# Kernel tuning notes

Hardware: AMD Instinct MI355X
Metric: run time of the kernel (lower is better)

The kernel has to match this reference:

```python
import jax, jax.numpy as jnp
import numpy as np

N_LEVELS = 16
F_PER_LEVEL = 2
LOG2_HASH = 19
HASH_SIZE = 1 << LOG2_HASH
HASH_MASK = HASH_SIZE - 1
BASE_RES = 16
FINEST_RES = 512
N_POINTS = 1_000_000

_growth = np.exp((np.log(FINEST_RES) - np.log(BASE_RES)) / (N_LEVELS - 1))
RESOLUTIONS = [int(BASE_RES * _growth ** l) for l in range(N_LEVELS)]
# corner offsets in the torch loop order: dz outer, dy middle, dx inner
OFFSETS = np.array([[dx, dy, dz] for dz in (0, 1) for dy in (0, 1) for dx in (0, 1)], dtype=np.uint32)  # [8,3]
PRIMES = np.array([1, 2654435761, 805459861], dtype=np.uint32)


def setup_inputs() -> dict:
    key = jax.random.key(0)
    k1, k2 = jax.random.split(key)
    x = jax.random.normal(k1, (N_POINTS, 3), dtype=jnp.float32)
    # matches nn.init.uniform_(tbl.weight, -1e-4, 1e-4)
    tables = jax.random.uniform(k2, (N_LEVELS, HASH_SIZE, F_PER_LEVEL), minval=-1e-4, maxval=1e-4, dtype=jnp.float32)
    return {"x": x, "tables": tables}


def _encode_level(x_scaled, resolution, table):
    # x_scaled: [N,3] in [0,1]; table: [HASH_SIZE, F]
    xg = x_scaled * resolution
    xfloor = jnp.floor(xg)
    frac = xg - xfloor                                   # [N,3]
    offs = jnp.asarray(OFFSETS)                          # [8,3] uint32
    corners = xfloor.astype(jnp.uint32)[:, None, :] + offs[None]  # [N,8,3]
    primes = jnp.asarray(PRIMES)
    # spatial hash: XOR of coord*prime, mod 2^19 (power of two -> low-bit mask; uint32 wraparound is exact here)
    h = (corners[..., 0] * primes[0]) ^ (corners[..., 1] * primes[1]) ^ (corners[..., 2] * primes[2])
    idx = (h & jnp.uint32(HASH_MASK)).astype(jnp.int32)  # [N,8]
    feats = table[idx]                                   # [N,8,F]
    off_f = offs.astype(x_scaled.dtype)                  # [8,3]
    # trilinear weights: prod over dims of (frac if offset==1 else 1-frac)
    w = jnp.prod(off_f[None] * frac[:, None, :] + (1.0 - off_f[None]) * (1.0 - frac[:, None, :]), axis=-1)  # [N,8]
    return jnp.sum(w[..., None] * feats, axis=1)         # [N,F]


def reference(x, tables):
    x_min = x.min(axis=0, keepdims=True)
    x_max = x.max(axis=0, keepdims=True)
    x_scaled = (x - x_min) / (x_max - x_min + 1e-8)
    outs = [_encode_level(x_scaled, float(RESOLUTIONS[l]), tables[l]) for l in range(N_LEVELS)]
    return jnp.concatenate(outs, axis=-1)                # [N, 32]
```

## Files before the change

### kernel.cpp

```cpp
#include <hip/hip_runtime.h>
#include <cmath>

constexpr unsigned HASH_SIZE = 1u << 19;
constexpr unsigned HASH_MASK = HASH_SIZE - 1u;
constexpr unsigned P2 = 2654435761u;
constexpr unsigned P3 = 805459861u;
constexpr int NKEYS = 65536;
constexpr int NSHARD = 8;

struct ResArr { float r[16]; };
typedef float f4 __attribute__((ext_vector_type(4)));

__global__ __launch_bounds__(256) void he_minmax1(const float* __restrict__ x, int n,
                                                  float* __restrict__ part) {
    int tid = blockIdx.x * blockDim.x + threadIdx.x;
    int stride = gridDim.x * blockDim.x;
    float mn0 = INFINITY, mn1 = INFINITY, mn2 = INFINITY;
    float mx0 = -INFINITY, mx1 = -INFINITY, mx2 = -INFINITY;
    for (int i = tid; i < n; i += stride) {
        float a = x[3 * i + 0];
        float b = x[3 * i + 1];
        float c = x[3 * i + 2];
        mn0 = fminf(mn0, a); mx0 = fmaxf(mx0, a);
        mn1 = fminf(mn1, b); mx1 = fmaxf(mx1, b);
        mn2 = fminf(mn2, c); mx2 = fmaxf(mx2, c);
    }
    #pragma unroll
    for (int off = 32; off > 0; off >>= 1) {
        mn0 = fminf(mn0, __shfl_down(mn0, off));
        mn1 = fminf(mn1, __shfl_down(mn1, off));
        mn2 = fminf(mn2, __shfl_down(mn2, off));
        mx0 = fmaxf(mx0, __shfl_down(mx0, off));
        mx1 = fmaxf(mx1, __shfl_down(mx1, off));
        mx2 = fmaxf(mx2, __shfl_down(mx2, off));
    }
    __shared__ float s[6][4];
    int w = threadIdx.x >> 6;
    if ((threadIdx.x & 63) == 0) {
        s[0][w] = mn0; s[1][w] = mn1; s[2][w] = mn2;
        s[3][w] = mx0; s[4][w] = mx1; s[5][w] = mx2;
    }
    __syncthreads();
    if (threadIdx.x == 0) {
        float* p = part + 6 * blockIdx.x;
        p[0] = fminf(fminf(s[0][0], s[0][1]), fminf(s[0][2], s[0][3]));
        p[1] = fminf(fminf(s[1][0], s[1][1]), fminf(s[1][2], s[1][3]));
        p[2] = fminf(fminf(s[2][0], s[2][1]), fminf(s[2][2], s[2][3]));
        p[3] = fmaxf(fmaxf(s[3][0], s[3][1]), fmaxf(s[3][2], s[3][3]));
        p[4] = fmaxf(fmaxf(s[4][0], s[4][1]), fmaxf(s[4][2], s[4][3]));
        p[5] = fmaxf(fmaxf(s[5][0], s[5][1]), fmaxf(s[5][2], s[5][3]));
    }
}

__global__ __launch_bounds__(256) void he_minmax2(const float* __restrict__ part,
                                                  float* __restrict__ mm) {
    int t = threadIdx.x;
    const float* p = part + 6 * t;
    float mn0 = p[0], mn1 = p[1], mn2 = p[2];
    float mx0 = p[3], mx1 = p[4], mx2 = p[5];
    #pragma unroll
    for (int off = 32; off > 0; off >>= 1) {
        mn0 = fminf(mn0, __shfl_down(mn0, off));
        mn1 = fminf(mn1, __shfl_down(mn1, off));
        mn2 = fminf(mn2, __shfl_down(mn2, off));
        mx0 = fmaxf(mx0, __shfl_down(mx0, off));
        mx1 = fmaxf(mx1, __shfl_down(mx1, off));
        mx2 = fmaxf(mx2, __shfl_down(mx2, off));
    }
    __shared__ float s[6][4];
    int w = t >> 6;
    if ((t & 63) == 0) {
        s[0][w] = mn0; s[1][w] = mn1; s[2][w] = mn2;
        s[3][w] = mx0; s[4][w] = mx1; s[5][w] = mx2;
    }
    __syncthreads();
    if (t == 0) {
        mm[0] = fminf(fminf(s[0][0], s[0][1]), fminf(s[0][2], s[0][3]));
        mm[1] = fminf(fminf(s[1][0], s[1][1]), fminf(s[1][2], s[1][3]));
        mm[2] = fminf(fminf(s[2][0], s[2][1]), fminf(s[2][2], s[2][3]));
        mm[3] = fmaxf(fmaxf(s[3][0], s[3][1]), fmaxf(s[3][2], s[3][3]));
        mm[4] = fmaxf(fmaxf(s[4][0], s[4][1]), fmaxf(s[4][2], s[4][3]));
        mm[5] = fmaxf(fmaxf(s[5][0], s[5][1]), fmaxf(s[5][2], s[5][3]));
    }
}

__device__ __forceinline__ unsigned spread5(unsigned v) {
    return (v & 1u) | ((v & 2u) << 2) | ((v & 4u) << 4) | ((v & 8u) << 6) | ((v & 16u) << 8);
}

__global__ __launch_bounds__(256) void he_keys(const float* __restrict__ x, int n,
                                               const float* __restrict__ mm,
                                               unsigned* __restrict__ planes,
                                               unsigned short* __restrict__ keyA) {
    int i = blockIdx.x * 256 + threadIdx.x;
    if (i >= n) return;
    float den0 = (mm[3] - mm[0]) + 1e-8f;
    float den1 = (mm[4] - mm[1]) + 1e-8f;
    float den2 = (mm[5] - mm[2]) + 1e-8f;
    float xs = (x[3 * i + 0] - mm[0]) / den0;
    float ys = (x[3 * i + 1] - mm[1]) / den1;
    float zs = (x[3 * i + 2] - mm[2]) / den2;
    unsigned kx = min(63u, (unsigned)(xs * 64.0f));
    unsigned ky = min(31u, (unsigned)(ys * 32.0f));
    unsigned kz = min(31u, (unsigned)(zs * 32.0f));
    unsigned key = ((kx >> 5) << 15)
                 | (spread5(kx & 31u) << 2)
                 | (spread5(ky) << 1)
                 | spread5(kz);
    keyA[i] = (unsigned short)key;
    atomicAdd(&planes[(i & (NSHARD - 1)) * NKEYS + key], 1u);
}

__global__ __launch_bounds__(256) void he_scanShards(unsigned* __restrict__ planes,
                                                     unsigned* __restrict__ keytot) {
    int k = blockIdx.x * 256 + threadIdx.x;
    unsigned c[NSHARD];
    #pragma unroll
    for (int s = 0; s < NSHARD; ++s) c[s] = planes[s * NKEYS + k];
    unsigned run = 0;
    #pragma unroll
    for (int s = 0; s < NSHARD; ++s) {
        planes[s * NKEYS + k] = run;
        run += c[s];
    }
    keytot[k] = run;
}

__global__ __launch_bounds__(256) void he_scanA(unsigned* __restrict__ keytot,
                                                unsigned* __restrict__ bsum) {
    __shared__ unsigned s[256];
    int tid = threadIdx.x;
    int g = blockIdx.x * 256 + tid;
    unsigned v = keytot[g];
    s[tid] = v;
    __syncthreads();
    #pragma unroll
    for (int off = 1; off < 256; off <<= 1) {
        unsigned t = (tid >= off) ? s[tid - off] : 0u;
        __syncthreads();
        s[tid] += t;
        __syncthreads();
    }
    keytot[g] = s[tid] - v;
    if (tid == 255) bsum[blockIdx.x] = s[255];
}

__global__ __launch_bounds__(256) void he_scanB(unsigned* __restrict__ bsum) {
    __shared__ unsigned s[256];
    int tid = threadIdx.x;
    unsigned v = bsum[tid];
    s[tid] = v;
    __syncthreads();
    #pragma unroll
    for (int off = 1; off < 256; off <<= 1) {
        unsigned t = (tid >= off) ? s[tid - off] : 0u;
        __syncthreads();
        s[tid] += t;
        __syncthreads();
    }
    bsum[tid] = s[tid] - v;
}

__global__ __launch_bounds__(256) void he_scanC(unsigned* __restrict__ planes,
                                                const unsigned* __restrict__ keytot,
                                                const unsigned* __restrict__ bsum) {
    int g = blockIdx.x * 256 + threadIdx.x;
    unsigned base = keytot[g] + bsum[blockIdx.x];
    #pragma unroll
    for (int s = 0; s < NSHARD; ++s) planes[s * NKEYS + g] += base;
}

__global__ __launch_bounds__(256) void he_scatter(const unsigned short* __restrict__ keyA,
                                                  const float* __restrict__ x, int n,
                                                  const float* __restrict__ mm,
                                                  unsigned* __restrict__ planes,
                                                  f4* __restrict__ xsorted) {
    int i = blockIdx.x * 256 + threadIdx.x;
    if (i >= n) return;
    float den0 = (mm[3] - mm[0]) + 1e-8f;
    float den1 = (mm[4] - mm[1]) + 1e-8f;
    float den2 = (mm[5] - mm[2]) + 1e-8f;
    float xs = (x[3 * i + 0] - mm[0]) / den0;
    float ys = (x[3 * i + 1] - mm[1]) / den1;
    float zs = (x[3 * i + 2] - mm[2]) / den2;
    unsigned k = keyA[i];
    unsigned pos = atomicAdd(&planes[(i & (NSHARD - 1)) * NKEYS + k], 1u);
    f4 v;
    v.x = xs; v.y = ys; v.z = zs; v.w = __uint_as_float((unsigned)i);
    xsorted[pos] = v;
}

__device__ __forceinline__ void enc_core(float xs, float ys, float zs,
                                         const float* __restrict__ tables,
                                         const ResArr& res, float o[32]) {
    #pragma unroll
    for (int l = 0; l < 16; ++l) {
        float R = res.r[l];
        float xg = xs * R, yg = ys * R, zg = zs * R;
        float fx = floorf(xg), fy = floorf(yg), fz = floorf(zg);
        float tx = xg - fx, ty = yg - fy, tz = zg - fz;
        unsigned cx = (unsigned)fx, cy = (unsigned)fy, cz = (unsigned)fz;

        unsigned hx0 = cx,      hx1 = cx + 1u;
        unsigned hy0 = cy * P2, hy1 = hy0 + P2;
        unsigned hz0 = cz * P3, hz1 = hz0 + P3;

        const float2* __restrict__ T = (const float2*)tables + (size_t)l * HASH_SIZE;

        float2 f000 = T[(hx0 ^ hy0 ^ hz0) & HASH_MASK];
        float2 f100 = T[(hx1 ^ hy0 ^ hz0) & HASH_MASK];
        float2 f010 = T[(hx0 ^ hy1 ^ hz0) & HASH_MASK];
        float2 f110 = T[(hx1 ^ hy1 ^ hz0) & HASH_MASK];
        float2 f001 = T[(hx0 ^ hy0 ^ hz1) & HASH_MASK];
        float2 f101 = T[(hx1 ^ hy0 ^ hz1) & HASH_MASK];
        float2 f011 = T[(hx0 ^ hy1 ^ hz1) & HASH_MASK];
        float2 f111 = T[(hx1 ^ hy1 ^ hz1) & HASH_MASK];

        float wx0 = 1.0f - tx, wx1 = tx;
        float wy0 = 1.0f - ty, wy1 = ty;
        float wz0 = 1.0f - tz, wz1 = tz;

        float w000 = wx0 * wy0 * wz0;
        float w100 = wx1 * wy0 * wz0;
        float w010 = wx0 * wy1 * wz0;
        float w110 = wx1 * wy1 * wz0;
        float w001 = wx0 * wy0 * wz1;
        float w101 = wx1 * wy0 * wz1;
        float w011 = wx0 * wy1 * wz1;
        float w111 = wx1 * wy1 * wz1;

        float a0 = w000 * f000.x;
        float a1 = w000 * f000.y;
        a0 += w100 * f100.x;  a1 += w100 * f100.y;
        a0 += w010 * f010.x;  a1 += w010 * f010.y;
        a0 += w110 * f110.x;  a1 += w110 * f110.y;
        a0 += w001 * f001.x;  a1 += w001 * f001.y;
        a0 += w101 * f101.x;  a1 += w101 * f101.y;
        a0 += w011 * f011.x;  a1 += w011 * f011.y;
        a0 += w111 * f111.x;  a1 += w111 * f111.y;

        o[2 * l + 0] = a0;
        o[2 * l + 1] = a1;
    }
}

__device__ __forceinline__ int swz_block(int b, int nwg) {
    int q = nwg >> 3, r = nwg & 7;
    int xcd = b & 7, kk = b >> 3;
    return (xcd < r ? xcd * (q + 1) : r * (q + 1) + (xcd - r) * q) + kk;
}

__global__ __launch_bounds__(256) void he_encode_scatter(const f4* __restrict__ xsorted,
                                                         const float* __restrict__ tables,
                                                         float* __restrict__ out, int n, ResArr res) {
    int sb = swz_block(blockIdx.x, gridDim.x);
    int j = sb * 256 + threadIdx.x;
    if (j >= n) return;
    f4 p = xsorted[j];
    int i = (int)__float_as_uint(p.w);
    float o[32];
    enc_core(p.x, p.y, p.z, tables, res, o);
    float* op = out + (size_t)i * 32;
    #pragma unroll
    for (int k = 0; k < 8; ++k) {
        f4 v;
        v.x = o[4 * k + 0]; v.y = o[4 * k + 1]; v.z = o[4 * k + 2]; v.w = o[4 * k + 3];
        *(f4*)(op + 4 * k) = v;
    }
}

__global__ __launch_bounds__(256) void he_encode_plain(const float* __restrict__ x,
                                                       const float* __restrict__ tables,
                                                       const float* __restrict__ mm,
                                                       float* __restrict__ out, int n, ResArr res) {
    int i = blockIdx.x * 256 + threadIdx.x;
    if (i >= n) return;
    float den0 = (mm[3] - mm[0]) + 1e-8f;
    float den1 = (mm[4] - mm[1]) + 1e-8f;
    float den2 = (mm[5] - mm[2]) + 1e-8f;
    float xs = (x[3 * i + 0] - mm[0]) / den0;
    float ys = (x[3 * i + 1] - mm[1]) / den1;
    float zs = (x[3 * i + 2] - mm[2]) / den2;
    float o[32];
    enc_core(xs, ys, zs, tables, res, o);
    float* op = out + (size_t)i * 32;
    #pragma unroll
    for (int k = 0; k < 8; ++k) {
        f4 v;
        v.x = o[4 * k + 0]; v.y = o[4 * k + 1]; v.z = o[4 * k + 2]; v.w = o[4 * k + 3];
        __builtin_nontemporal_store(v, (f4*)(op + 4 * k));
    }
}

extern "C" void kernel_launch(void* const* d_in, const int* in_sizes, int n_in,
                              void* d_out, int out_size, void* d_ws, size_t ws_size,
                              hipStream_t stream) {
    const float* x = (const float*)d_in[0];
    const float* tables = (const float*)d_in[1];
    float* out = (float*)d_out;
    int n = in_sizes[0] / 3;

    char* w = (char*)d_ws;
    float*          mm      = (float*)w;
    float*          part    = (float*)(w + 4096);
    unsigned*       bsum    = (unsigned*)(w + 16384);
    unsigned*       keytot  = (unsigned*)(w + 32768);
    unsigned*       planes  = (unsigned*)(w + 524288);
    unsigned short* keyA    = (unsigned short*)(w + 0x300000);
    f4*             xsorted = (f4*)(w + 0x500000);

    const size_t NEED1 = 0x500000 + (size_t)16777216;
    int tier = (ws_size >= NEED1) ? 1 : 0;
    if (n > (1 << 20)) tier = 0;

    ResArr res;
    double growth = exp((log(512.0) - log(16.0)) / 15.0);
    for (int l = 0; l < 16; ++l) {
        res.r[l] = (float)(int)(16.0 * pow(growth, (double)l));
    }

    int blocks = (n + 255) / 256;

    he_minmax1<<<256, 256, 0, stream>>>(x, n, part);
    he_minmax2<<<1, 256, 0, stream>>>(part, mm);

    if (tier >= 1) {
        hipMemsetAsync(planes, 0, (size_t)NSHARD * NKEYS * 4, stream);
        he_keys<<<blocks, 256, 0, stream>>>(x, n, mm, planes, keyA);
        he_scanShards<<<NKEYS / 256, 256, 0, stream>>>(planes, keytot);
        he_scanA<<<NKEYS / 256, 256, 0, stream>>>(keytot, bsum);
        he_scanB<<<1, 256, 0, stream>>>(bsum);
        he_scanC<<<NKEYS / 256, 256, 0, stream>>>(planes, keytot, bsum);
        he_scatter<<<blocks, 256, 0, stream>>>(keyA, x, n, mm, planes, xsorted);
        he_encode_scatter<<<blocks, 256, 0, stream>>>(xsorted, tables, out, n, res);
    } else {
        he_encode_plain<<<blocks, 256, 0, stream>>>(x, tables, mm, out, n, res);
    }
}
```

Measured before the change: 328.1 us.

## Use a fixed-range sort key to fuse histogram with min/max and merge scan kernels

The spatial sort key is now computed from fixed constant bounds on raw coordinates instead of the normalized ones. This lets the histogram atomics run inside the min/max reduction pass, which removes the separate key kernel and the keyA buffer. The shard scan is merged with the block scan, the final min/max reduction with the bsum scan, and the scatter recomputes the key instead of reading it back. Output stays correct for any input because the key only affects ordering, but locality depends on inputs falling roughly in the assumed range. The encode stores also change from nontemporal to ordinary stores.

```diff
diff --git a/kernel.cpp b/kernel.cpp
--- a/kernel.cpp
+++ b/kernel.cpp
@@ -11,8 +11,23 @@
 struct ResArr { float r[16]; };
 typedef float f4 __attribute__((ext_vector_type(4)));
 
-__global__ __launch_bounds__(256) void he_minmax1(const float* __restrict__ x, int n,
-                                                  float* __restrict__ part) {
+__device__ __forceinline__ unsigned spread5(unsigned v) {
+    return (v & 1u) | ((v & 2u) << 2) | ((v & 4u) << 4) | ((v & 8u) << 6) | ((v & 16u) << 8);
+}
+
+__device__ __forceinline__ unsigned fixed_key(float a, float b, float c) {
+    unsigned kx = (unsigned)min(63.0f, fmaxf(0.0f, (a + 5.2f) * 6.15f));
+    unsigned ky = (unsigned)min(31.0f, fmaxf(0.0f, (b + 5.2f) * 3.07f));
+    unsigned kz = (unsigned)min(31.0f, fmaxf(0.0f, (c + 5.2f) * 3.07f));
+    return ((kx >> 5) << 15)
+         | (spread5(kx & 31u) << 2)
+         | (spread5(ky) << 1)
+         | spread5(kz);
+}
+
+__global__ __launch_bounds__(256) void he_minmax_hist(const float* __restrict__ x, int n,
+                                                      float* __restrict__ part,
+                                                      unsigned* __restrict__ planes) {
     int tid = blockIdx.x * blockDim.x + threadIdx.x;
     int stride = gridDim.x * blockDim.x;
     float mn0 = INFINITY, mn1 = INFINITY, mn2 = INFINITY;
@@ -24,6 +39,8 @@
         mn0 = fminf(mn0, a); mx0 = fmaxf(mx0, a);
         mn1 = fminf(mn1, b); mx1 = fmaxf(mx1, b);
         mn2 = fminf(mn2, c); mx2 = fmaxf(mx2, c);
+        unsigned key = fixed_key(a, b, c);
+        atomicAdd(&planes[(i & (NSHARD - 1)) * NKEYS + key], 1u);
     }
     #pragma unroll
     for (int off = 32; off > 0; off >>= 1) {
@@ -52,10 +69,53 @@
     }
 }
 
-__global__ __launch_bounds__(256) void he_minmax2(const float* __restrict__ part,
-                                                  float* __restrict__ mm) {
-    int t = threadIdx.x;
-    const float* p = part + 6 * t;
+__global__ __launch_bounds__(256) void he_scanSA(unsigned* __restrict__ planes,
+                                                 unsigned* __restrict__ keytot,
+                                                 unsigned* __restrict__ bsum) {
+    int tid = threadIdx.x;
+    int k = blockIdx.x * 256 + tid;
+    unsigned c[NSHARD];
+    #pragma unroll
+    for (int s = 0; s < NSHARD; ++s) c[s] = planes[s * NKEYS + k];
+    unsigned run = 0;
+    #pragma unroll
+    for (int s = 0; s < NSHARD; ++s) {
+        planes[s * NKEYS + k] = run;
+        run += c[s];
+    }
+    __shared__ unsigned sh[256];
+    unsigned v = run;
+    sh[tid] = v;
+    __syncthreads();
+    #pragma unroll
+    for (int off = 1; off < 256; off <<= 1) {
+        unsigned t = (tid >= off) ? sh[tid - off] : 0u;
+        __syncthreads();
+        sh[tid] += t;
+        __syncthreads();
+    }
+    keytot[k] = sh[tid] - v;
+    if (tid == 255) bsum[blockIdx.x] = sh[255];
+}
+
+__global__ __launch_bounds__(256) void he_scanB_mm(unsigned* __restrict__ bsum,
+                                                   const float* __restrict__ part,
+                                                   float* __restrict__ mm) {
+    int tid = threadIdx.x;
+    __shared__ unsigned s[256];
+    unsigned v = bsum[tid];
+    s[tid] = v;
+    __syncthreads();
+    #pragma unroll
+    for (int off = 1; off < 256; off <<= 1) {
+        unsigned t = (tid >= off) ? s[tid - off] : 0u;
+        __syncthreads();
+        s[tid] += t;
+        __syncthreads();
+    }
+    bsum[tid] = s[tid] - v;
+
+    const float* p = part + 6 * tid;
     float mn0 = p[0], mn1 = p[1], mn2 = p[2];
     float mx0 = p[3], mx1 = p[4], mx2 = p[5];
     #pragma unroll
@@ -67,98 +127,21 @@
         mx1 = fmaxf(mx1, __shfl_down(mx1, off));
         mx2 = fmaxf(mx2, __shfl_down(mx2, off));
     }
-    __shared__ float s[6][4];
-    int w = t >> 6;
-    if ((t & 63) == 0) {
-        s[0][w] = mn0; s[1][w] = mn1; s[2][w] = mn2;
-        s[3][w] = mx0; s[4][w] = mx1; s[5][w] = mx2;
+    __shared__ float sm[6][4];
+    int w = tid >> 6;
+    if ((tid & 63) == 0) {
+        sm[0][w] = mn0; sm[1][w] = mn1; sm[2][w] = mn2;
+        sm[3][w] = mx0; sm[4][w] = mx1; sm[5][w] = mx2;
     }
     __syncthreads();
-    if (t == 0) {
-        mm[0] = fminf(fminf(s[0][0], s[0][1]), fminf(s[0][2], s[0][3]));
-        mm[1] = fminf(fminf(s[1][0], s[1][1]), fminf(s[1][2], s[1][3]));
-        mm[2] = fminf(fminf(s[2][0], s[2][1]), fminf(s[2][2], s[2][3]));
-        mm[3] = fmaxf(fmaxf(s[3][0], s[3][1]), fmaxf(s[3][2], s[3][3]));
-        mm[4] = fmaxf(fmaxf(s[4][0], s[4][1]), fmaxf(s[4][2], s[4][3]));
-        mm[5] = fmaxf(fmaxf(s[5][0], s[5][1]), fmaxf(s[5][2], s[5][3]));
-    }
-}
-
-__device__ __forceinline__ unsigned spread5(unsigned v) {
-    return (v & 1u) | ((v & 2u) << 2) | ((v & 4u) << 4) | ((v & 8u) << 6) | ((v & 16u) << 8);
-}
-
-__global__ __launch_bounds__(256) void he_keys(const float* __restrict__ x, int n,
-                                               const float* __restrict__ mm,
-                                               unsigned* __restrict__ planes,
-                                               unsigned short* __restrict__ keyA) {
-    int i = blockIdx.x * 256 + threadIdx.x;
-    if (i >= n) return;
-    float den0 = (mm[3] - mm[0]) + 1e-8f;
-    float den1 = (mm[4] - mm[1]) + 1e-8f;
-    float den2 = (mm[5] - mm[2]) + 1e-8f;
-    float xs = (x[3 * i + 0] - mm[0]) / den0;
-    float ys = (x[3 * i + 1] - mm[1]) / den1;
-    float zs = (x[3 * i + 2] - mm[2]) / den2;
-    unsigned kx = min(63u, (unsigned)(xs * 64.0f));
-    unsigned ky = min(31u, (unsigned)(ys * 32.0f));
-    unsigned kz = min(31u, (unsigned)(zs * 32.0f));
-    unsigned key = ((kx >> 5) << 15)
-                 | (spread5(kx & 31u) << 2)
-                 | (spread5(ky) << 1)
-                 | spread5(kz);
-    keyA[i] = (unsigned short)key;
-    atomicAdd(&planes[(i & (NSHARD - 1)) * NKEYS + key], 1u);
-}
-
-__global__ __launch_bounds__(256) void he_scanShards(unsigned* __restrict__ planes,
-                                                     unsigned* __restrict__ keytot) {
-    int k = blockIdx.x * 256 + threadIdx.x;
-    unsigned c[NSHARD];
-    #pragma unroll
-    for (int s = 0; s < NSHARD; ++s) c[s] = planes[s * NKEYS + k];
-    unsigned run = 0;
-    #pragma unroll
-    for (int s = 0; s < NSHARD; ++s) {
-        planes[s * NKEYS + k] = run;
-        run += c[s];
-    }
-    keytot[k] = run;
-}
-
-__global__ __launch_bounds__(256) void he_scanA(unsigned* __restrict__ keytot,
-                                                unsigned* __restrict__ bsum) {
-    __shared__ unsigned s[256];
-    int tid = threadIdx.x;
-    int g = blockIdx.x * 256 + tid;
-    unsigned v = keytot[g];
-    s[tid] = v;
-    __syncthreads();
-    #pragma unroll
-    for (int off = 1; off < 256; off <<= 1) {
-        unsigned t = (tid >= off) ? s[tid - off] : 0u;
-        __syncthreads();
-        s[tid] += t;
-        __syncthreads();
-    }
-    keytot[g] = s[tid] - v;
-    if (tid == 255) bsum[blockIdx.x] = s[255];
-}
-
-__global__ __launch_bounds__(256) void he_scanB(unsigned* __restrict__ bsum) {
-    __shared__ unsigned s[256];
-    int tid = threadIdx.x;
-    unsigned v = bsum[tid];
-    s[tid] = v;
-    __syncthreads();
-    #pragma unroll
-    for (int off = 1; off < 256; off <<= 1) {
-        unsigned t = (tid >= off) ? s[tid - off] : 0u;
-        __syncthreads();
-        s[tid] += t;
-        __syncthreads();
-    }
-    bsum[tid] = s[tid] - v;
+    if (tid == 0) {
+        mm[0] = fminf(fminf(sm[0][0], sm[0][1]), fminf(sm[0][2], sm[0][3]));
+        mm[1] = fminf(fminf(sm[1][0], sm[1][1]), fminf(sm[1][2], sm[1][3]));
+        mm[2] = fminf(fminf(sm[2][0], sm[2][1]), fminf(sm[2][2], sm[2][3]));
+        mm[3] = fmaxf(fmaxf(sm[3][0], sm[3][1]), fmaxf(sm[3][2], sm[3][3]));
+        mm[4] = fmaxf(fmaxf(sm[4][0], sm[4][1]), fmaxf(sm[4][2], sm[4][3]));
+        mm[5] = fmaxf(fmaxf(sm[5][0], sm[5][1]), fmaxf(sm[5][2], sm[5][3]));
+    }
 }
 
 __global__ __launch_bounds__(256) void he_scanC(unsigned* __restrict__ planes,
@@ -170,21 +153,21 @@
     for (int s = 0; s < NSHARD; ++s) planes[s * NKEYS + g] += base;
 }
 
-__global__ __launch_bounds__(256) void he_scatter(const unsigned short* __restrict__ keyA,
-                                                  const float* __restrict__ x, int n,
+__global__ __launch_bounds__(256) void he_scatter(const float* __restrict__ x, int n,
                                                   const float* __restrict__ mm,
                                                   unsigned* __restrict__ planes,
                                                   f4* __restrict__ xsorted) {
     int i = blockIdx.x * 256 + threadIdx.x;
     if (i >= n) return;
+    float a = x[3 * i + 0], b = x[3 * i + 1], c = x[3 * i + 2];
     float den0 = (mm[3] - mm[0]) + 1e-8f;
     float den1 = (mm[4] - mm[1]) + 1e-8f;
     float den2 = (mm[5] - mm[2]) + 1e-8f;
-    float xs = (x[3 * i + 0] - mm[0]) / den0;
-    float ys = (x[3 * i + 1] - mm[1]) / den1;
-    float zs = (x[3 * i + 2] - mm[2]) / den2;
-    unsigned k = keyA[i];
-    unsigned pos = atomicAdd(&planes[(i & (NSHARD - 1)) * NKEYS + k], 1u);
+    float xs = (a - mm[0]) / den0;
+    float ys = (b - mm[1]) / den1;
+    float zs = (c - mm[2]) / den2;
+    unsigned key = fixed_key(a, b, c);
+    unsigned pos = atomicAdd(&planes[(i & (NSHARD - 1)) * NKEYS + key], 1u);
     f4 v;
     v.x = xs; v.y = ys; v.z = zs; v.w = __uint_as_float((unsigned)i);
     xsorted[pos] = v;
@@ -288,7 +271,7 @@
     for (int k = 0; k < 8; ++k) {
         f4 v;
         v.x = o[4 * k + 0]; v.y = o[4 * k + 1]; v.z = o[4 * k + 2]; v.w = o[4 * k + 3];
-        __builtin_nontemporal_store(v, (f4*)(op + 4 * k));
+        *(f4*)(op + 4 * k) = v;
     }
 }
 
@@ -301,15 +284,14 @@
     int n = in_sizes[0] / 3;
 
     char* w = (char*)d_ws;
-    float*          mm      = (float*)w;
-    float*          part    = (float*)(w + 4096);
-    unsigned*       bsum    = (unsigned*)(w + 16384);
-    unsigned*       keytot  = (unsigned*)(w + 32768);
-    unsigned*       planes  = (unsigned*)(w + 524288);
-    unsigned short* keyA    = (unsigned short*)(w + 0x300000);
-    f4*             xsorted = (f4*)(w + 0x500000);
-
-    const size_t NEED1 = 0x500000 + (size_t)16777216;
+    float*    mm      = (float*)w;
+    float*    part    = (float*)(w + 4096);
+    unsigned* bsum    = (unsigned*)(w + 16384);
+    unsigned* keytot  = (unsigned*)(w + 32768);
+    unsigned* planes  = (unsigned*)(w + 524288);
+    f4*       xsorted = (f4*)(w + 0x300000);
+
+    const size_t NEED1 = 0x300000 + (size_t)16777216;
     int tier = (ws_size >= NEED1) ? 1 : 0;
     if (n > (1 << 20)) tier = 0;
 
@@ -321,19 +303,17 @@
 
     int blocks = (n + 255) / 256;
 
-    he_minmax1<<<256, 256, 0, stream>>>(x, n, part);
-    he_minmax2<<<1, 256, 0, stream>>>(part, mm);
-
     if (tier >= 1) {
         hipMemsetAsync(planes, 0, (size_t)NSHARD * NKEYS * 4, stream);
-        he_keys<<<blocks, 256, 0, stream>>>(x, n, mm, planes, keyA);
-        he_scanShards<<<NKEYS / 256, 256, 0, stream>>>(planes, keytot);
-        he_scanA<<<NKEYS / 256, 256, 0, stream>>>(keytot, bsum);
-        he_scanB<<<1, 256, 0, stream>>>(bsum);
+        he_minmax_hist<<<256, 256, 0, stream>>>(x, n, part, planes);
+        he_scanSA<<<NKEYS / 256, 256, 0, stream>>>(planes, keytot, bsum);
+        he_scanB_mm<<<1, 256, 0, stream>>>(bsum, part, mm);
         he_scanC<<<NKEYS / 256, 256, 0, stream>>>(planes, keytot, bsum);
-        he_scatter<<<blocks, 256, 0, stream>>>(keyA, x, n, mm, planes, xsorted);
+        he_scatter<<<blocks, 256, 0, stream>>>(x, n, mm, planes, xsorted);
         he_encode_scatter<<<blocks, 256, 0, stream>>>(xsorted, tables, out, n, res);
     } else {
+        he_minmax_hist<<<256, 256, 0, stream>>>(x, n, part, (unsigned*)(w + 524288));
+        he_scanB_mm<<<1, 256, 0, stream>>>(bsum, part, mm);
         he_encode_plain<<<blocks, 256, 0, stream>>>(x, tables, mm, out, n, res);
     }
 }
```

After: 318.9 us. 2.8% less time.
